# Kernel optimization log

Hardware: AMD Instinct MI355X
Metric: run time of the kernel (lower is better)

The kernel has to match this reference:

```python
import jax, jax.numpy as jnp
import numpy as np


def setup_inputs() -> dict:
    key = jax.random.key(0)
    ks = jax.random.split(key, 8)
    N, F, H, B = 500_000, 128, 64, 1024
    x1 = jax.random.normal(ks[0], (N, F), dtype=jnp.float32)
    x2 = jax.random.normal(ks[1], (N, F), dtype=jnp.float32)
    batch1 = jax.random.randint(ks[2], (N,), 0, B, dtype=jnp.int32)
    batch2 = jax.random.randint(ks[3], (N,), 0, B, dtype=jnp.int32)
    # attn_mlp params: Linear(F->H), tanh, Linear(H->1)
    W1 = jax.random.normal(ks[4], (F, H), dtype=jnp.float32) * (1.0 / np.sqrt(F))
    b1 = jnp.zeros((H,), dtype=jnp.float32)
    W2 = jax.random.normal(ks[5], (H, 1), dtype=jnp.float32) * (1.0 / np.sqrt(H))
    b2 = jnp.zeros((1,), dtype=jnp.float32)
    return dict(x1=x1, x2=x2, batch1=batch1, batch2=batch2, B=B,
                W1=W1, b1=b1, W2=W2, b2=b2)


def _attn_pool(x, batch, B, W1, b1, W2, b2):
    # score = attn_mlp(x).squeeze(-1)  : [N]
    score = (jnp.tanh(x @ W1 + b1) @ W2 + b2)[:, 0]
    # per-graph (segment) softmax, numerically stable
    m = jax.ops.segment_max(score, batch, num_segments=B)      # [B]
    e = jnp.exp(score - m[batch])                               # [N]
    s = jax.ops.segment_sum(e, batch, num_segments=B)           # [B]
    attn = e / s[batch]                                         # [N]
    # dropout is identity in eval mode
    # scatter-sum pooling of attn-weighted features
    return jax.ops.segment_sum(attn[:, None] * x, batch, num_segments=B)  # [B, F]


def reference(x1, x2, batch1, batch2, B, W1, b1, W2, b2):
    p1 = _attn_pool(x1, batch1, B, W1, b1, W2, b2)
    p2 = _attn_pool(x2, batch2, B, W1, b1, W2, b2)
    # mean over node types (stack(...).mean(0))
    return 0.5 * (p1 + p2)
```

## Files before the change

kernel.cpp:

```cpp
#include <hip/hip_runtime.h>
#include <hip/hip_bf16.h>
#include <math.h>

#define NF 128
#define NH 64
#define NB 1024
#define CAP 768
#define SPAD 16
#define LDSW 136

struct NodeW { int idx; float w; };

typedef __attribute__((ext_vector_type(8))) short short8;
typedef __attribute__((ext_vector_type(4))) float f32x4;

static __device__ inline short f2bf(float f) {
    __hip_bfloat16 h = __float2bfloat16(f);
    short r; __builtin_memcpy(&r, &h, 2); return r;
}

static __device__ inline float tanh_fast(float a) {
    float t = __expf(-2.0f * fabsf(a));
    float th = (1.0f - t) / (1.0f + t);
    return copysignf(th, a);
}

__global__ __launch_bounds__(256) void mtap_prep(
    const float* __restrict__ W1, const float* __restrict__ W2,
    const float* __restrict__ bias2, unsigned short* __restrict__ w1t,
    float* __restrict__ mconst)
{
    int tid = threadIdx.x;
    #pragma unroll
    for (int i = 0; i < 32; ++i) {
        int L = tid + i * 256;
        int n = L >> 7, k = L & 127;
        w1t[L] = (unsigned short)f2bf(W1[k * NH + n]);
    }
    if (tid < 64) {
        float v = fabsf(W2[tid]);
        #pragma unroll
        for (int off = 32; off >= 1; off >>= 1) v += __shfl_down(v, off);
        if (tid == 0) mconst[0] = v + fabsf(bias2[0]);
    }
}

__global__ __launch_bounds__(256) void mtap_init(float* __restrict__ s,
                                                 int* __restrict__ cursor) {
    int i = blockIdx.x * 256 + threadIdx.x;
    if (i < 2 * NB * SPAD) { s[i] = 0.0f; cursor[i] = 0; }
}

__global__ __launch_bounds__(256) void mtap_score(
    const float* __restrict__ x1, const float* __restrict__ x2,
    const int* __restrict__ g1, const int* __restrict__ g2,
    const unsigned short* __restrict__ w1t, const float* __restrict__ bias1,
    const float* __restrict__ W2, const float* __restrict__ bias2,
    const float* __restrict__ mconst,
    int* __restrict__ cursor, NodeW* __restrict__ bins,
    float* __restrict__ s_arr, int N)
{
    __shared__ unsigned short w1lds[64 * LDSW];
    int tid = threadIdx.x;

    #pragma unroll
    for (int i = 0; i < 4; ++i) {
        int lin = tid * 4 + i;
        int n = lin >> 4, c16 = lin & 15;
        short8 v = *(const short8*)(w1t + lin * 8);
        *(short8*)&w1lds[n * LDSW + c16 * 8] = v;
    }
    __syncthreads();

    int lane = tid & 63, w = tid >> 6;
    int c = lane & 15, q = lane >> 4;
    long twoN = 2L * N;
    long base = (long)blockIdx.x * 128 + w * 32;

    const float* rp[2];
    #pragma unroll
    for (int a = 0; a < 2; ++a) {
        long r = base + a * 16 + c;
        if (r >= twoN) r = twoN - 1;
        rp[a] = (r >= N) ? (x2 + (r - N) * NF) : (x1 + r * NF);
    }

    f32x4 acc[2][4];
    float w2v[4];
    #pragma unroll
    for (int t = 0; t < 4; ++t) {
        float bv = bias1[t * 16 + c];
        w2v[t] = W2[t * 16 + c];
        #pragma unroll
        for (int a = 0; a < 2; ++a) acc[a][t] = f32x4{bv, bv, bv, bv};
    }

    #pragma unroll
    for (int s = 0; s < 4; ++s) {
        short8 af[2];
        #pragma unroll
        for (int a = 0; a < 2; ++a) {
            const float4* p = (const float4*)(rp[a] + s * 32 + q * 8);
            float4 f0 = p[0], f1 = p[1];
            af[a] = short8{f2bf(f0.x), f2bf(f0.y), f2bf(f0.z), f2bf(f0.w),
                           f2bf(f1.x), f2bf(f1.y), f2bf(f1.z), f2bf(f1.w)};
        }
        #pragma unroll
        for (int t = 0; t < 4; ++t) {
            short8 bf8 = *(const short8*)&w1lds[(t * 16 + c) * LDSW + s * 32 + q * 8];
            acc[0][t] = __builtin_amdgcn_mfma_f32_16x16x32_bf16(af[0], bf8, acc[0][t], 0, 0, 0);
            acc[1][t] = __builtin_amdgcn_mfma_f32_16x16x32_bf16(af[1], bf8, acc[1][t], 0, 0, 0);
        }
    }

    float p2[8];
    #pragma unroll
    for (int a = 0; a < 2; ++a)
        #pragma unroll
        for (int r = 0; r < 4; ++r) {
            float p = 0.0f;
            #pragma unroll
            for (int t = 0; t < 4; ++t)
                p = fmaf(tanh_fast(acc[a][t][r]), w2v[t], p);
            p2[a * 4 + r] = p;
        }
    #pragma unroll
    for (int m = 1; m <= 8; m <<= 1)
        #pragma unroll
        for (int k = 0; k < 8; ++k)
            p2[k] += __shfl_xor(p2[k], m);

    if (c < 8) {
        float sv = p2[0];
        #pragma unroll
        for (int k = 1; k < 8; ++k) sv = (c == k) ? p2[k] : sv;
        int a = c >> 2, r = c & 3;
        long gid = base + a * 16 + q * 4 + r;
        if (gid < twoN) {
            int ty = gid >= N;
            int n = ty ? (int)(gid - N) : (int)gid;
            int seg = (ty ? g2 : g1)[n];
            int bin = ty * NB + seg;
            float e = __expf(sv + bias2[0] - mconst[0]);
            int pos = atomicAdd(&cursor[bin * SPAD], 1);
            if (pos < CAP) bins[(long)bin * CAP + pos] = NodeW{n, e};
            atomicAdd(&s_arr[bin * SPAD], e);
        }
    }
}

__global__ __launch_bounds__(256) void mtap_accum(
    const float* __restrict__ x1, const float* __restrict__ x2,
    const NodeW* __restrict__ bins, const int* __restrict__ cursor,
    const float* __restrict__ s_arr, float* __restrict__ out)
{
    int seg = blockIdx.x;
    int wv = threadIdx.x >> 6;
    int lane = threadIdx.x & 63;
    float ox = 0.0f, oy = 0.0f;

    #pragma unroll
    for (int ty = 0; ty < 2; ++ty) {
        int bin = ty * NB + seg;
        const float* x = ty ? x2 : x1;
        int cnt = min(cursor[bin * SPAD], CAP);
        float ssum = s_arr[bin * SPAD];
        float scale = (cnt > 0) ? 0.5f / ssum : 0.0f;
        const NodeW* b = bins + (long)bin * CAP;
        float ax = 0.0f, ay = 0.0f;
        int j = wv;
        for (; j + 28 < cnt; j += 32) {
            NodeW pp[8];
            float2 vv[8];
            #pragma unroll
            for (int u = 0; u < 8; ++u) pp[u] = b[j + 4 * u];
            #pragma unroll
            for (int u = 0; u < 8; ++u)
                vv[u] = *(const float2*)(x + (long)pp[u].idx * NF + 2 * lane);
            #pragma unroll
            for (int u = 0; u < 8; ++u) {
                ax = fmaf(pp[u].w, vv[u].x, ax);
                ay = fmaf(pp[u].w, vv[u].y, ay);
            }
        }
        for (; j < cnt; j += 4) {
            NodeW p = b[j];
            float2 v = *(const float2*)(x + (long)p.idx * NF + 2 * lane);
            ax = fmaf(p.w, v.x, ax);
            ay = fmaf(p.w, v.y, ay);
        }
        ox = fmaf(scale, ax, ox);
        oy = fmaf(scale, ay, oy);
    }

    __shared__ float red[4][NF];
    *(float2*)&red[wv][2 * lane] = make_float2(ox, oy);
    __syncthreads();
    int t = threadIdx.x;
    if (t < NF)
        out[seg * NF + t] = red[0][t] + red[1][t] + red[2][t] + red[3][t];
}

extern "C" void kernel_launch(void* const* d_in, const int* in_sizes, int n_in,
                              void* d_out, int out_size, void* d_ws, size_t ws_size,
                              hipStream_t stream)
{
    const float* x1    = (const float*)d_in[0];
    const float* x2    = (const float*)d_in[1];
    const int*   g1    = (const int*)d_in[2];
    const int*   g2    = (const int*)d_in[3];
    const float* W1    = (const float*)d_in[5];
    const float* bias1 = (const float*)d_in[6];
    const float* W2    = (const float*)d_in[7];
    const float* bias2 = (const float*)d_in[8];
    int N = in_sizes[2];

    char* wsp = (char*)d_ws;
    NodeW* bins = (NodeW*)wsp;                 wsp += (size_t)2 * NB * CAP * sizeof(NodeW);
    float* s_arr = (float*)wsp;                wsp += (size_t)2 * NB * SPAD * sizeof(float);
    int* cursor = (int*)wsp;                   wsp += (size_t)2 * NB * SPAD * sizeof(int);
    unsigned short* w1t = (unsigned short*)wsp; wsp += (size_t)NF * NH * sizeof(unsigned short);
    float* mconst = (float*)wsp;
    float* out = (float*)d_out;

    hipLaunchKernelGGL(mtap_prep, dim3(1), dim3(256), 0, stream,
                       W1, W2, bias2, w1t, mconst);
    hipLaunchKernelGGL(mtap_init, dim3((2 * NB * SPAD + 255) / 256), dim3(256), 0,
                       stream, s_arr, cursor);
    long twoN = 2L * N;
    int nb = (int)((twoN + 127) / 128);
    hipLaunchKernelGGL(mtap_score, dim3(nb), dim3(256), 0, stream,
                       x1, x2, g1, g2, w1t, bias1, W2, bias2, mconst,
                       cursor, bins, s_arr, N);
    hipLaunchKernelGGL(mtap_accum, dim3(NB), dim3(256), 0, stream,
                       x1, x2, bins, cursor, s_arr, out);
}
```

Measured before the change: 655.3 us.

## Make score kernel persistent with W1 fragments held in registers

The score kernel becomes a grid-stride persistent kernel with a fixed grid of 1024 blocks. Each wave loads its W1 bf16 fragments from LDS into registers once and reuses them for every 32-row tile, and the bias loads are hoisted out of the loop. This removes the per-block LDS staging of W1 and the repeated LDS reads for each tile. In exchange it holds 64 extra VGPRs per lane for the fragments under a two-block launch bound, and tanh now uses a fast divide. With fewer waves there is less parallelism available to hide memory latency in this streaming, memory-bound pass.

```diff
diff --git a/kernel.cpp b/kernel.cpp
--- a/kernel.cpp
+++ b/kernel.cpp
@@ -21,7 +21,7 @@
 
 static __device__ inline float tanh_fast(float a) {
     float t = __expf(-2.0f * fabsf(a));
-    float th = (1.0f - t) / (1.0f + t);
+    float th = __fdividef(1.0f - t, 1.0f + t);
     return copysignf(th, a);
 }
 
@@ -51,7 +51,7 @@
     if (i < 2 * NB * SPAD) { s[i] = 0.0f; cursor[i] = 0; }
 }
 
-__global__ __launch_bounds__(256) void mtap_score(
+__global__ __launch_bounds__(256, 2) void mtap_score(
     const float* __restrict__ x1, const float* __restrict__ x2,
     const int* __restrict__ g1, const int* __restrict__ g2,
     const unsigned short* __restrict__ w1t, const float* __restrict__ bias1,
@@ -74,77 +74,92 @@
 
     int lane = tid & 63, w = tid >> 6;
     int c = lane & 15, q = lane >> 4;
+
+    short8 bfrag[4][4];
+    #pragma unroll
+    for (int t = 0; t < 4; ++t)
+        #pragma unroll
+        for (int s = 0; s < 4; ++s)
+            bfrag[t][s] = *(const short8*)&w1lds[(t * 16 + c) * LDSW + s * 32 + q * 8];
+
+    float b1v[4], w2v[4];
+    #pragma unroll
+    for (int t = 0; t < 4; ++t) {
+        b1v[t] = bias1[t * 16 + c];
+        w2v[t] = W2[t * 16 + c];
+    }
+    float shift = bias2[0] - mconst[0];
+
     long twoN = 2L * N;
-    long base = (long)blockIdx.x * 128 + w * 32;
-
-    const float* rp[2];
-    #pragma unroll
-    for (int a = 0; a < 2; ++a) {
-        long r = base + a * 16 + c;
-        if (r >= twoN) r = twoN - 1;
-        rp[a] = (r >= N) ? (x2 + (r - N) * NF) : (x1 + r * NF);
-    }
-
-    f32x4 acc[2][4];
-    float w2v[4];
-    #pragma unroll
-    for (int t = 0; t < 4; ++t) {
-        float bv = bias1[t * 16 + c];
-        w2v[t] = W2[t * 16 + c];
-        #pragma unroll
-        for (int a = 0; a < 2; ++a) acc[a][t] = f32x4{bv, bv, bv, bv};
-    }
-
-    #pragma unroll
-    for (int s = 0; s < 4; ++s) {
-        short8 af[2];
+    int gw = blockIdx.x * 4 + w;
+    long step = (long)gridDim.x * 4 * 32;
+
+    for (long base = (long)gw * 32; base < twoN; base += step) {
+        const float* rp[2];
         #pragma unroll
         for (int a = 0; a < 2; ++a) {
-            const float4* p = (const float4*)(rp[a] + s * 32 + q * 8);
-            float4 f0 = p[0], f1 = p[1];
-            af[a] = short8{f2bf(f0.x), f2bf(f0.y), f2bf(f0.z), f2bf(f0.w),
-                           f2bf(f1.x), f2bf(f1.y), f2bf(f1.z), f2bf(f1.w)};
-        }
-        #pragma unroll
-        for (int t = 0; t < 4; ++t) {
-            short8 bf8 = *(const short8*)&w1lds[(t * 16 + c) * LDSW + s * 32 + q * 8];
-            acc[0][t] = __builtin_amdgcn_mfma_f32_16x16x32_bf16(af[0], bf8, acc[0][t], 0, 0, 0);
-            acc[1][t] = __builtin_amdgcn_mfma_f32_16x16x32_bf16(af[1], bf8, acc[1][t], 0, 0, 0);
-        }
-    }
-
-    float p2[8];
-    #pragma unroll
-    for (int a = 0; a < 2; ++a)
-        #pragma unroll
-        for (int r = 0; r < 4; ++r) {
-            float p = 0.0f;
-            #pragma unroll
-            for (int t = 0; t < 4; ++t)
-                p = fmaf(tanh_fast(acc[a][t][r]), w2v[t], p);
-            p2[a * 4 + r] = p;
-        }
-    #pragma unroll
-    for (int m = 1; m <= 8; m <<= 1)
-        #pragma unroll
-        for (int k = 0; k < 8; ++k)
-            p2[k] += __shfl_xor(p2[k], m);
-
-    if (c < 8) {
-        float sv = p2[0];
-        #pragma unroll
-        for (int k = 1; k < 8; ++k) sv = (c == k) ? p2[k] : sv;
-        int a = c >> 2, r = c & 3;
-        long gid = base + a * 16 + q * 4 + r;
-        if (gid < twoN) {
-            int ty = gid >= N;
-            int n = ty ? (int)(gid - N) : (int)gid;
-            int seg = (ty ? g2 : g1)[n];
-            int bin = ty * NB + seg;
-            float e = __expf(sv + bias2[0] - mconst[0]);
-            int pos = atomicAdd(&cursor[bin * SPAD], 1);
-            if (pos < CAP) bins[(long)bin * CAP + pos] = NodeW{n, e};
-            atomicAdd(&s_arr[bin * SPAD], e);
+            long r = base + a * 16 + c;
+            if (r >= twoN) r = twoN - 1;
+            rp[a] = (r >= N) ? (x2 + (r - N) * NF) : (x1 + r * NF);
+        }
+
+        f32x4 acc[2][4];
+        #pragma unroll
+        for (int t = 0; t < 4; ++t)
+            #pragma unroll
+            for (int a = 0; a < 2; ++a)
+                acc[a][t] = f32x4{b1v[t], b1v[t], b1v[t], b1v[t]};
+
+        #pragma unroll
+        for (int s = 0; s < 4; ++s) {
+            short8 af[2];
+            #pragma unroll
+            for (int a = 0; a < 2; ++a) {
+                const float4* p = (const float4*)(rp[a] + s * 32 + q * 8);
+                float4 f0 = p[0], f1 = p[1];
+                af[a] = short8{f2bf(f0.x), f2bf(f0.y), f2bf(f0.z), f2bf(f0.w),
+                               f2bf(f1.x), f2bf(f1.y), f2bf(f1.z), f2bf(f1.w)};
+            }
+            #pragma unroll
+            for (int t = 0; t < 4; ++t) {
+                acc[0][t] = __builtin_amdgcn_mfma_f32_16x16x32_bf16(af[0], bfrag[t][s], acc[0][t], 0, 0, 0);
+                acc[1][t] = __builtin_amdgcn_mfma_f32_16x16x32_bf16(af[1], bfrag[t][s], acc[1][t], 0, 0, 0);
+            }
+        }
+
+        float p2[8];
+        #pragma unroll
+        for (int a = 0; a < 2; ++a)
+            #pragma unroll
+            for (int r = 0; r < 4; ++r) {
+                float p = 0.0f;
+                #pragma unroll
+                for (int t = 0; t < 4; ++t)
+                    p = fmaf(tanh_fast(acc[a][t][r]), w2v[t], p);
+                p2[a * 4 + r] = p;
+            }
+        #pragma unroll
+        for (int m = 1; m <= 8; m <<= 1)
+            #pragma unroll
+            for (int k = 0; k < 8; ++k)
+                p2[k] += __shfl_xor(p2[k], m);
+
+        if (c < 8) {
+            float sv = p2[0];
+            #pragma unroll
+            for (int k = 1; k < 8; ++k) sv = (c == k) ? p2[k] : sv;
+            int a = c >> 2, r = c & 3;
+            long gid = base + a * 16 + q * 4 + r;
+            if (gid < twoN) {
+                int ty = gid >= N;
+                int n = ty ? (int)(gid - N) : (int)gid;
+                int seg = (ty ? g2 : g1)[n];
+                int bin = ty * NB + seg;
+                float e = __expf(sv + shift);
+                int pos = atomicAdd(&cursor[bin * SPAD], 1);
+                if (pos < CAP) bins[(long)bin * CAP + pos] = NodeW{n, e};
+                atomicAdd(&s_arr[bin * SPAD], e);
+            }
         }
     }
 }
@@ -227,9 +242,7 @@
                        W1, W2, bias2, w1t, mconst);
     hipLaunchKernelGGL(mtap_init, dim3((2 * NB * SPAD + 255) / 256), dim3(256), 0,
                        stream, s_arr, cursor);
-    long twoN = 2L * N;
-    int nb = (int)((twoN + 127) / 128);
-    hipLaunchKernelGGL(mtap_score, dim3(nb), dim3(256), 0, stream,
+    hipLaunchKernelGGL(mtap_score, dim3(1024), dim3(256), 0, stream,
                        x1, x2, g1, g2, w1t, bias1, W2, bias2, mconst,
                        cursor, bins, s_arr, N);
     hipLaunchKernelGGL(mtap_accum, dim3(NB), dim3(256), 0, stream,
```

New measurement: 654.5 us. About the same (-0.1%).
